# Kernel tuning notes

Measured on AMD Instinct MI355X. Metric: run time of the kernel, lower is better.

Reference implementation:

```python
import jax, jax.numpy as jnp
import numpy as np

N_NODES = 50000
N_HEADS = 8
CH = 32  # channels per degree for both key and value
NUM_KEY_FEATS = CH * 1 + CH * 3  # sum over degrees t of ch*(2t+1) = 128


def setup_inputs() -> dict:
    key = jax.random.key(0)
    ks = jax.random.split(key, 7)
    E = 800000
    return {
        "q0": jax.random.normal(ks[0], (N_NODES, CH, 1), dtype=jnp.float32),
        "q1": jax.random.normal(ks[1], (N_NODES, CH, 3), dtype=jnp.float32),
        "k0": jax.random.normal(ks[2], (E, CH, 1), dtype=jnp.float32),
        "k1": jax.random.normal(ks[3], (E, CH, 3), dtype=jnp.float32),
        "v0": jax.random.normal(ks[4], (E, CH, 1), dtype=jnp.float32),
        "v1": jax.random.normal(ks[5], (E, CH, 3), dtype=jnp.float32),
        "edge_dst": jax.random.randint(ks[6], (E,), 0, N_NODES, dtype=jnp.int64),
    }


def _edge_softmax(e, dst, n_nodes):
    # e: [E, H] scores; softmax over edges sharing the same destination node
    m = jax.ops.segment_max(e, dst, num_segments=n_nodes)  # [N, H]
    ex = jnp.exp(e - m[dst])
    denom = jax.ops.segment_sum(ex, dst, num_segments=n_nodes)  # [N, H]
    return ex / denom[dst]


def reference(q0, q1, k0, k1, v0, v1, edge_dst):
    E = k0.shape[0]
    H = N_HEADS
    # keys/queries: view [*, ch, 2t+1] -> [*, H, ch//H*(2t+1)], concat over degrees
    khat = jnp.concatenate(
        [k0.reshape(E, H, -1), k1.reshape(E, H, -1)], axis=-1)  # [E, H, D]
    qhat = jnp.concatenate(
        [q0.reshape(N_NODES, H, -1), q1.reshape(N_NODES, H, -1)], axis=-1)  # [N, H, D]
    # e_dot_v: edge key dot destination-node query
    e = jnp.einsum('ehd,ehd->eh', khat, qhat[edge_dst])  # [E, H]
    e = e / np.sqrt(NUM_KEY_FEATS).astype(np.float32)
    a = _edge_softmax(e, edge_dst, N_NODES)  # [E, H]
    # weighted scatter-sum of values per degree
    outs = []
    for v, t in ((v0, 0), (v1, 1)):
        vh = v.reshape(E, H, CH // H, 2 * t + 1)
        msg = a[:, :, None, None] * vh  # [E, H, ch/H, 2t+1]
        agg = jax.ops.segment_sum(msg, edge_dst, num_segments=N_NODES)
        outs.append(agg.reshape(N_NODES, CH, 2 * t + 1))
    return tuple(outs)
```

## Files before the change

### kernel.cpp

```cpp
#include <hip/hip_runtime.h>
#include <cstddef>

#define NN 50000
#define WAVES_PER_BLOCK 4

__global__ void hist_kernel(const int* __restrict__ dst, int* __restrict__ counts, int E) {
    int i = blockIdx.x * blockDim.x + threadIdx.x;
    if (i < E) atomicAdd(&counts[dst[i]], 1);
}

__global__ void scan_kernel(const int* __restrict__ counts, int* __restrict__ offsets,
                            int* __restrict__ cursor, int n) {
    const int T = 1024;
    int t = threadIdx.x;
    int chunk = (n + T - 1) / T;
    int begin = t * chunk;
    int end = begin + chunk; if (end > n) end = n;

    int s = 0;
    for (int i = begin; i < end; ++i) s += counts[i];

    __shared__ int sums[T];
    sums[t] = s;
    __syncthreads();
    for (int off = 1; off < T; off <<= 1) {
        int v = (t >= off) ? sums[t - off] : 0;
        __syncthreads();
        sums[t] += v;
        __syncthreads();
    }
    int run = (t == 0) ? 0 : sums[t - 1];
    for (int i = begin; i < end; ++i) {
        offsets[i] = run;
        cursor[i]  = run;
        run += counts[i];
    }
    if (t == T - 1) offsets[n] = run;
}

__global__ void scatter_kernel(const int* __restrict__ dst, int* __restrict__ cursor,
                               int* __restrict__ sorted, int E) {
    int i = blockIdx.x * blockDim.x + threadIdx.x;
    if (i < E) {
        int d = dst[i];
        int pos = atomicAdd(&cursor[d], 1);
        sorted[pos] = i;
    }
}

__global__ __launch_bounds__(256) void attn_kernel(
    const float* __restrict__ q0, const float* __restrict__ q1,
    const float* __restrict__ k0, const float* __restrict__ k1,
    const float* __restrict__ v0, const float* __restrict__ v1,
    const int* __restrict__ offsets, const int* __restrict__ sorted,
    float* __restrict__ out)
{
    int wave = threadIdx.x >> 6;
    int node = blockIdx.x * WAVES_PER_BLOCK + wave;
    if (node >= NN) return;
    int lane = threadIdx.x & 63;
    int h  = lane & 7;
    int es = lane >> 3;

    const float4 qa = *(const float4*)(q0 + (size_t)node * 32 + 4 * h);
    const float4* q1p = (const float4*)(q1 + (size_t)node * 96 + 12 * h);
    const float4 qb = q1p[0], qc = q1p[1], qd = q1p[2];

    int rs = offsets[node], re = offsets[node + 1];

    float acc[16];
#pragma unroll
    for (int j = 0; j < 16; ++j) acc[j] = 0.f;
    float l = 0.f;

    for (int base = rs; base < re; base += 8) {
        int ei = base + es;
        bool valid = ei < re;
        int e = sorted[valid ? ei : rs];

        const float4 ka = *(const float4*)(k0 + (size_t)e * 32 + 4 * h);
        const float4* k1p = (const float4*)(k1 + (size_t)e * 96 + 12 * h);
        const float4 kb = k1p[0], kc = k1p[1], kd = k1p[2];

        float s = qa.x * ka.x + qa.y * ka.y + qa.z * ka.z + qa.w * ka.w
                + qb.x * kb.x + qb.y * kb.y + qb.z * kb.z + qb.w * kb.w
                + qc.x * kc.x + qc.y * kc.y + qc.z * kc.z + qc.w * kc.w
                + qd.x * kd.x + qd.y * kd.y + qd.z * kd.z + qd.w * kd.w;

        float w = valid ? __expf(s * 0.08838834764831845f) : 0.f;
        l += w;

        const float4 va = *(const float4*)(v0 + (size_t)e * 32 + 4 * h);
        const float4* v1p = (const float4*)(v1 + (size_t)e * 96 + 12 * h);
        const float4 vb = v1p[0], vc = v1p[1], vd = v1p[2];

        acc[0]  += w * va.x; acc[1]  += w * va.y; acc[2]  += w * va.z; acc[3]  += w * va.w;
        acc[4]  += w * vb.x; acc[5]  += w * vb.y; acc[6]  += w * vb.z; acc[7]  += w * vb.w;
        acc[8]  += w * vc.x; acc[9]  += w * vc.y; acc[10] += w * vc.z; acc[11] += w * vc.w;
        acc[12] += w * vd.x; acc[13] += w * vd.y; acc[14] += w * vd.z; acc[15] += w * vd.w;
    }

#pragma unroll
    for (int m = 8; m < 64; m <<= 1) {
        l += __shfl_xor(l, m, 64);
#pragma unroll
        for (int j = 0; j < 16; ++j) acc[j] += __shfl_xor(acc[j], m, 64);
    }

    if (es == 0) {
        float r = (l > 0.f) ? (1.0f / l) : 0.f;
        float4 o0; o0.x = acc[0] * r; o0.y = acc[1] * r; o0.z = acc[2] * r; o0.w = acc[3] * r;
        *(float4*)(out + (size_t)node * 32 + 4 * h) = o0;
        float* o1 = out + (size_t)NN * 32 + (size_t)node * 96 + 12 * h;
        float4 t0; t0.x = acc[4]  * r; t0.y = acc[5]  * r; t0.z = acc[6]  * r; t0.w = acc[7]  * r;
        float4 t1; t1.x = acc[8]  * r; t1.y = acc[9]  * r; t1.z = acc[10] * r; t1.w = acc[11] * r;
        float4 t2; t2.x = acc[12] * r; t2.y = acc[13] * r; t2.z = acc[14] * r; t2.w = acc[15] * r;
        ((float4*)o1)[0] = t0;
        ((float4*)o1)[1] = t1;
        ((float4*)o1)[2] = t2;
    }
}

extern "C" void kernel_launch(void* const* d_in, const int* in_sizes, int n_in,
                              void* d_out, int out_size, void* d_ws, size_t ws_size,
                              hipStream_t stream) {
    const float* q0 = (const float*)d_in[0];
    const float* q1 = (const float*)d_in[1];
    const float* k0 = (const float*)d_in[2];
    const float* k1 = (const float*)d_in[3];
    const float* v0 = (const float*)d_in[4];
    const float* v1 = (const float*)d_in[5];
    const int*  dst = (const int*)d_in[6];
    const int E = in_sizes[6];
    float* out = (float*)d_out;

    int* offsets = (int*)d_ws;
    int* cursor  = offsets + (NN + 1);
    int* counts  = cursor + NN;
    int* sorted  = counts + NN;

    hipMemsetAsync(counts, 0, NN * sizeof(int), stream);
    hist_kernel<<<(E + 255) / 256, 256, 0, stream>>>(dst, counts, E);
    scan_kernel<<<1, 1024, 0, stream>>>(counts, offsets, cursor, NN);
    scatter_kernel<<<(E + 255) / 256, 256, 0, stream>>>(dst, cursor, sorted, E);
    attn_kernel<<<(NN + WAVES_PER_BLOCK - 1) / WAVES_PER_BLOCK, 256, 0, stream>>>(
        q0, q1, k0, k1, v0, v1, offsets, sorted, out);
}
```

Measured before the change: 932.1 us.

## Replace single-block scan with multi-block scan and rank-based placement

Replaces the single-block serial prefix scan over node counts with a three-stage multi-block scan built from wave shuffles. The histogram pass now records each edge's atomic rank, so the placement pass computes positions directly from offsets plus rank without a second round of atomics. This targets the latency of the serial scan and the contended cursor atomics, at the cost of extra kernel launches and a rank buffer of size E.

After: 795.5 us. 1.17x faster.

```diff
diff --git a/kernel.cpp b/kernel.cpp
--- a/kernel.cpp
+++ b/kernel.cpp
@@ -2,49 +2,79 @@
 #include <cstddef>
 
 #define NN 50000
-#define WAVES_PER_BLOCK 4
+#define WPB 4
+#define SCAN_B 256
+#define NB1 ((NN + SCAN_B - 1) / SCAN_B)
 
-__global__ void hist_kernel(const int* __restrict__ dst, int* __restrict__ counts, int E) {
-    int i = blockIdx.x * blockDim.x + threadIdx.x;
-    if (i < E) atomicAdd(&counts[dst[i]], 1);
+__device__ __forceinline__ int block_inc_scan(int x, int* lds) {
+    int lane = threadIdx.x & 63;
+    int wid  = threadIdx.x >> 6;
+#pragma unroll
+    for (int d = 1; d < 64; d <<= 1) {
+        int v = __shfl_up(x, d, 64);
+        if (lane >= d) x += v;
+    }
+    if (lane == 63) lds[wid] = x;
+    __syncthreads();
+    if (wid == 0 && lane < 4) {
+        int s = lds[lane];
+#pragma unroll
+        for (int d = 1; d < 4; d <<= 1) {
+            int v = __shfl_up(s, d, 64);
+            if (lane >= d) s += v;
+        }
+        lds[lane] = s;
+    }
+    __syncthreads();
+    if (wid > 0) x += lds[wid - 1];
+    return x;
 }
 
-__global__ void scan_kernel(const int* __restrict__ counts, int* __restrict__ offsets,
-                            int* __restrict__ cursor, int n) {
-    const int T = 1024;
-    int t = threadIdx.x;
-    int chunk = (n + T - 1) / T;
-    int begin = t * chunk;
-    int end = begin + chunk; if (end > n) end = n;
-
-    int s = 0;
-    for (int i = begin; i < end; ++i) s += counts[i];
-
-    __shared__ int sums[T];
-    sums[t] = s;
-    __syncthreads();
-    for (int off = 1; off < T; off <<= 1) {
-        int v = (t >= off) ? sums[t - off] : 0;
-        __syncthreads();
-        sums[t] += v;
-        __syncthreads();
-    }
-    int run = (t == 0) ? 0 : sums[t - 1];
-    for (int i = begin; i < end; ++i) {
-        offsets[i] = run;
-        cursor[i]  = run;
-        run += counts[i];
-    }
-    if (t == T - 1) offsets[n] = run;
-}
-
-__global__ void scatter_kernel(const int* __restrict__ dst, int* __restrict__ cursor,
-                               int* __restrict__ sorted, int E) {
+__global__ void hist_rank_kernel(const int* __restrict__ dst, int* __restrict__ counts,
+                                 int* __restrict__ rank, int E) {
     int i = blockIdx.x * blockDim.x + threadIdx.x;
     if (i < E) {
         int d = dst[i];
-        int pos = atomicAdd(&cursor[d], 1);
-        sorted[pos] = i;
+        rank[i] = atomicAdd(&counts[d], 1);
+    }
+}
+
+__global__ __launch_bounds__(SCAN_B) void scan_sum_kernel(const int* __restrict__ counts,
+                                                          int* __restrict__ bsum) {
+    __shared__ int lds[4];
+    int i = blockIdx.x * SCAN_B + threadIdx.x;
+    int c = (i < NN) ? counts[i] : 0;
+    int inc = block_inc_scan(c, lds);
+    if (threadIdx.x == SCAN_B - 1) bsum[blockIdx.x] = inc;
+}
+
+__global__ __launch_bounds__(SCAN_B) void scan_base_kernel(const int* __restrict__ bsum,
+                                                           int* __restrict__ bbase,
+                                                           int* __restrict__ offsets) {
+    __shared__ int lds[4];
+    int t = threadIdx.x;
+    int c = (t < NB1) ? bsum[t] : 0;
+    int inc = block_inc_scan(c, lds);
+    if (t < NB1) bbase[t] = inc - c;
+    if (t == NB1 - 1) offsets[NN] = inc;
+}
+
+__global__ __launch_bounds__(SCAN_B) void scan_off_kernel(const int* __restrict__ counts,
+                                                          const int* __restrict__ bbase,
+                                                          int* __restrict__ offsets) {
+    __shared__ int lds[4];
+    int i = blockIdx.x * SCAN_B + threadIdx.x;
+    int c = (i < NN) ? counts[i] : 0;
+    int inc = block_inc_scan(c, lds);
+    if (i < NN) offsets[i] = bbase[blockIdx.x] + inc - c;
+}
+
+__global__ void place_kernel(const int* __restrict__ dst, const int* __restrict__ rank,
+                             const int* __restrict__ offsets, int* __restrict__ sorted, int E) {
+    int i = blockIdx.x * blockDim.x + threadIdx.x;
+    if (i < E) {
+        int d = dst[i];
+        sorted[offsets[d] + rank[i]] = i;
     }
 }
 
@@ -56,7 +86,7 @@
     float* __restrict__ out)
 {
     int wave = threadIdx.x >> 6;
-    int node = blockIdx.x * WAVES_PER_BLOCK + wave;
+    int node = blockIdx.x * WPB + wave;
     if (node >= NN) return;
     int lane = threadIdx.x & 63;
     int h  = lane & 7;
@@ -135,14 +165,18 @@
     float* out = (float*)d_out;
 
     int* offsets = (int*)d_ws;
-    int* cursor  = offsets + (NN + 1);
-    int* counts  = cursor + NN;
-    int* sorted  = counts + NN;
+    int* counts  = offsets + (NN + 1);
+    int* bsum    = counts + NN;
+    int* bbase   = bsum + NB1;
+    int* rank    = bbase + NB1;
+    int* sorted  = rank + E;
 
     hipMemsetAsync(counts, 0, NN * sizeof(int), stream);
-    hist_kernel<<<(E + 255) / 256, 256, 0, stream>>>(dst, counts, E);
-    scan_kernel<<<1, 1024, 0, stream>>>(counts, offsets, cursor, NN);
-    scatter_kernel<<<(E + 255) / 256, 256, 0, stream>>>(dst, cursor, sorted, E);
-    attn_kernel<<<(NN + WAVES_PER_BLOCK - 1) / WAVES_PER_BLOCK, 256, 0, stream>>>(
+    hist_rank_kernel<<<(E + 255) / 256, 256, 0, stream>>>(dst, counts, rank, E);
+    scan_sum_kernel<<<NB1, SCAN_B, 0, stream>>>(counts, bsum);
+    scan_base_kernel<<<1, SCAN_B, 0, stream>>>(bsum, bbase, offsets);
+    scan_off_kernel<<<NB1, SCAN_B, 0, stream>>>(counts, bbase, offsets);
+    place_kernel<<<(E + 255) / 256, 256, 0, stream>>>(dst, rank, offsets, sorted, E);
+    attn_kernel<<<(NN + WPB - 1) / WPB, 256, 0, stream>>>(
         q0, q1, k0, k1, v0, v1, offsets, sorted, out);
 }
```
